# Optimization experiments

Measured on AMD Instinct MI355X. Metric: run time of the kernel, lower is better.

Reference implementation:

```python
import jax, jax.numpy as jnp
import numpy as np

TEMPERATURE = 0.07
EPS = 1e-12  # matches F.normalize eps clamp


def setup_inputs() -> dict:
    key = jax.random.key(0)
    k1, k2 = jax.random.split(key)
    B, S, D = 8, 512, 128
    return {
        "z_i": jax.random.normal(k1, (B, S, D), dtype=jnp.float32),
        "z_j": jax.random.normal(k2, (B, S, D), dtype=jnp.float32),
    }


def reference(z_i, z_j):
    D = z_i.shape[-1]
    zi = z_i.reshape(-1, D)  # [N, D]
    zj = z_j.reshape(-1, D)
    # cosine normalization (use_cosine_similarity=True)
    zi = zi / jnp.maximum(jnp.linalg.norm(zi, axis=1, keepdims=True), EPS)
    zj = zj / jnp.maximum(jnp.linalg.norm(zj, axis=1, keepdims=True), EPS)
    N = zi.shape[0]
    z = jnp.concatenate([zi, zj], axis=0)  # [2N, D]
    sim = (z @ z.T) / TEMPERATURE  # [2N, 2N]
    # denominator: logsumexp over all j != i (positives + negatives)
    diag = jnp.eye(2 * N, dtype=bool)
    lse = jax.nn.logsumexp(jnp.where(diag, -jnp.inf, sim), axis=1)  # [2N]
    # positive logit for row i is sim[i, (i+N) mod 2N] = <zi, zj>/T for both halves
    pos_half = jnp.sum(zi * zj, axis=1) / TEMPERATURE  # [N]
    pos = jnp.concatenate([pos_half, pos_half])  # [2N]
    return jnp.mean(-pos + lse)
```

## Files before the change

### kernel.cpp

```cpp
#include <hip/hip_runtime.h>
#include <stdint.h>


#define TOTAL   8192
#define NHALF   4096
#define DK      128
#define TEMP_INV 14.285714285714286f
#define SCALE    4.539816f

#define JSPLITS 16
#define JCHUNK  (TOTAL / JSPLITS)
#define BN      64
#define NSTAGE  (JCHUNK / BN)
#define BM      256

typedef short  bf16x8  __attribute__((ext_vector_type(8)));
typedef float  floatx4 __attribute__((ext_vector_type(4)));

#if __has_builtin(__builtin_amdgcn_exp2f)
#define EXP2(x) __builtin_amdgcn_exp2f(x)
#else
#define EXP2(x) exp2f(x)
#endif

__device__ __forceinline__ uint32_t f2bf(float f) {
  uint32_t u = __float_as_uint(f);
  return (u + 0x7fffu + ((u >> 16) & 1u)) >> 16;
}
__device__ __forceinline__ uint32_t pack2bf(float lo, float hi) {
  return f2bf(lo) | (f2bf(hi) << 16);
}

__global__ __launch_bounds__(256) void ntx_norm(
    const float* __restrict__ zi, const float* __restrict__ zj,
    uint32_t* __restrict__ zn,
    float* __restrict__ pos,
    float* __restrict__ rowsum)
{
  const int t = threadIdx.x;
  if (blockIdx.x < 32) rowsum[blockIdx.x * 256 + t] = 0.0f;

  const int wave = t >> 6, lane = t & 63;
  const int i = blockIdx.x * 4 + wave;

  const float2 vi = *(const float2*)(zi + (size_t)i * DK + lane * 2);
  const float2 vj = *(const float2*)(zj + (size_t)i * DK + lane * 2);
  float ssi = vi.x * vi.x + vi.y * vi.y;
  float ssj = vj.x * vj.x + vj.y * vj.y;
  float dij = vi.x * vj.x + vi.y * vj.y;
#pragma unroll
  for (int m = 1; m <= 32; m <<= 1) {
    ssi += __shfl_xor(ssi, m, 64);
    ssj += __shfl_xor(ssj, m, 64);
    dij += __shfl_xor(dij, m, 64);
  }
  const float invi = 1.0f / fmaxf(sqrtf(ssi), 1e-12f);
  const float invj = 1.0f / fmaxf(sqrtf(ssj), 1e-12f);

  zn[(size_t)i * 64 + lane] =
      pack2bf(vi.x * invi * SCALE, vi.y * invi * SCALE);
  zn[(size_t)(i + NHALF) * 64 + lane] =
      pack2bf(vj.x * invj * SCALE, vj.y * invj * SCALE);
  if (lane == 0) pos[i] = dij * invi * invj * TEMP_INV;
}

__global__ __launch_bounds__(256, 2) void ntx_gemm(
    const uint16_t* __restrict__ z,
    float* __restrict__ rowsum)
{
  __shared__ uint4 lb4[BN * 17];

  const int t = threadIdx.x;
  const int wave = t >> 6, lane = t & 63;
  const int q = lane >> 4, c = lane & 15;
  const int i0 = blockIdx.x * BM;
  const int j0 = blockIdx.y * JCHUNK;
  const int rowbase = i0 + wave * 64;

  bf16x8 afrag[4][4];
#pragma unroll
  for (int s = 0; s < 4; ++s) {
    const uint16_t* ap = z + (size_t)(rowbase + s * 16 + c) * DK + q * 8;
#pragma unroll
    for (int kk = 0; kk < 4; ++kk)
      afrag[s][kk] = *(const bf16x8*)(ap + kk * 32);
  }

  float runsum[4][4];
#pragma unroll
  for (int s = 0; s < 4; ++s)
#pragma unroll
    for (int r = 0; r < 4; ++r) runsum[s][r] = 0.0f;

  const int ch = t & 15;
  const int r0 = t >> 4;

  for (int st = 0; st < NSTAGE; ++st) {
    const int jst = j0 + st * BN;
    __syncthreads();
#pragma unroll
    for (int p = 0; p < 4; ++p) {
      const int r = r0 + p * 16;
      uint4 v = *(const uint4*)(z + (size_t)(jst + r) * DK + ch * 8);
      lb4[r * 17 + ch] = v;
    }
    __syncthreads();

#pragma unroll
    for (int jt = 0; jt < BN / 16; ++jt) {
      bf16x8 bfrag[4];
#pragma unroll
      for (int kk = 0; kk < 4; ++kk)
        bfrag[kk] = *(const bf16x8*)&lb4[(jt * 16 + c) * 17 + kk * 4 + q];
      const int jc = jst + jt * 16;

#pragma unroll
      for (int s = 0; s < 4; ++s) {
        floatx4 acc = {0.0f, 0.0f, 0.0f, 0.0f};
#pragma unroll
        for (int kk = 0; kk < 4; ++kk)
          acc = __builtin_amdgcn_mfma_f32_16x16x32_bf16(afrag[s][kk],
                                                        bfrag[kk], acc,
                                                        0, 0, 0);
        const int rb = rowbase + s * 16;
        if (jc == rb) {
#pragma unroll
          for (int r = 0; r < 4; ++r) {
            float e = EXP2(acc[r]);
            runsum[s][r] += (q * 4 + r == c) ? 0.0f : e;
          }
        } else {
#pragma unroll
          for (int r = 0; r < 4; ++r) runsum[s][r] += EXP2(acc[r]);
        }
      }
    }
  }

#pragma unroll
  for (int s = 0; s < 4; ++s)
#pragma unroll
    for (int r = 0; r < 4; ++r) {
      float v = runsum[s][r];
      v += __shfl_xor(v, 1, 64);
      v += __shfl_xor(v, 2, 64);
      v += __shfl_xor(v, 4, 64);
      v += __shfl_xor(v, 8, 64);
      runsum[s][r] = v;
    }
  if (c == 0) {
#pragma unroll
    for (int s = 0; s < 4; ++s)
#pragma unroll
      for (int r = 0; r < 4; ++r)
        atomicAdd(&rowsum[rowbase + s * 16 + q * 4 + r], runsum[s][r]);
  }
}

__global__ __launch_bounds__(1024) void ntx_final(
    const float* __restrict__ rowsum, const float* __restrict__ pos,
    float* __restrict__ out)
{
  const int t = threadIdx.x;
  float acc = 0.0f;
  for (int r = t; r < TOTAL; r += 1024) acc += __logf(rowsum[r]);
  for (int r = t; r < NHALF; r += 1024) acc -= 2.0f * pos[r];
#pragma unroll
  for (int m = 1; m <= 32; m <<= 1) acc += __shfl_xor(acc, m, 64);
  __shared__ float red[16];
  const int wave = t >> 6, lane = t & 63;
  if (lane == 0) red[wave] = acc;
  __syncthreads();
  if (t == 0) {
    float s = 0.0f;
#pragma unroll
    for (int w = 0; w < 16; ++w) s += red[w];
    out[0] = s / (float)TOTAL;
  }
}

extern "C" void kernel_launch(void* const* d_in, const int* in_sizes, int n_in,
                              void* d_out, int out_size, void* d_ws,
                              size_t ws_size, hipStream_t stream) {
  const float* zi = (const float*)d_in[0];
  const float* zj = (const float*)d_in[1];
  float* out = (float*)d_out;

  char* ws = (char*)d_ws;
  uint16_t* zn     = (uint16_t*)ws;
  float*    rowsum = (float*)(ws + (size_t)TOTAL * DK * 2);
  float*    pos    = (float*)(ws + (size_t)TOTAL * DK * 2 + TOTAL * 4);

  ntx_norm<<<dim3(NHALF / 4), dim3(256), 0, stream>>>(zi, zj, (uint32_t*)zn,
                                                      pos, rowsum);
  ntx_gemm<<<dim3(TOTAL / BM, JSPLITS), dim3(256), 0, stream>>>(zn, rowsum);
  ntx_final<<<dim3(1), dim3(1024), 0, stream>>>(rowsum, pos, out);
}
```

Baseline: 86.35 us.

## Exploit similarity-matrix symmetry: compute upper-triangle tiles and scatter column sums

The GEMM+exp kernel now uses 128x128 tiles and computes only the tiles on or above the diagonal, since the similarity matrix is symmetric. Each off-diagonal tile adds its exp values both to its own rows and, through per-column partial sums, to the mirrored rows. The goal is to roughly halve the MFMA and exp2 work. In exchange it launches a 64x64 grid where about half the blocks exit at once, does a separate LDS load and sync per small tile, and issues many more global atomics, including duplicate column atomics from each of the four waves.

```diff
diff --git a/kernel.cpp b/kernel.cpp
--- a/kernel.cpp
+++ b/kernel.cpp
@@ -7,12 +7,7 @@
 #define DK      128
 #define TEMP_INV 14.285714285714286f
 #define SCALE    4.539816f
-
-#define JSPLITS 16
-#define JCHUNK  (TOTAL / JSPLITS)
-#define BN      64
-#define NSTAGE  (JCHUNK / BN)
-#define BM      256
+#define TILE    128
 
 typedef short  bf16x8  __attribute__((ext_vector_type(8)));
 typedef float  floatx4 __attribute__((ext_vector_type(4)));
@@ -64,81 +59,84 @@
   if (lane == 0) pos[i] = dij * invi * invj * TEMP_INV;
 }
 
-__global__ __launch_bounds__(256, 2) void ntx_gemm(
+__global__ __launch_bounds__(256, 4) void ntx_gemm(
     const uint16_t* __restrict__ z,
     float* __restrict__ rowsum)
 {
-  __shared__ uint4 lb4[BN * 17];
+  const int bi = blockIdx.x, bj = blockIdx.y;
+  if (bj < bi) return;
+
+  __shared__ uint4 lb4[TILE * 17];
 
   const int t = threadIdx.x;
   const int wave = t >> 6, lane = t & 63;
   const int q = lane >> 4, c = lane & 15;
-  const int i0 = blockIdx.x * BM;
-  const int j0 = blockIdx.y * JCHUNK;
-  const int rowbase = i0 + wave * 64;
-
-  bf16x8 afrag[4][4];
-#pragma unroll
-  for (int s = 0; s < 4; ++s) {
+  const int I0 = bi * TILE, J0 = bj * TILE;
+  const int rowbase = I0 + wave * 32;
+  const bool diagblk = (bi == bj);
+
+  {
+    const int ch = t & 15, r0 = t >> 4;
+#pragma unroll
+    for (int p = 0; p < 8; ++p) {
+      const int r = r0 + p * 16;
+      lb4[r * 17 + ch] = *(const uint4*)(z + (size_t)(J0 + r) * DK + ch * 8);
+    }
+  }
+
+  bf16x8 afrag[2][4];
+#pragma unroll
+  for (int s = 0; s < 2; ++s) {
     const uint16_t* ap = z + (size_t)(rowbase + s * 16 + c) * DK + q * 8;
 #pragma unroll
     for (int kk = 0; kk < 4; ++kk)
       afrag[s][kk] = *(const bf16x8*)(ap + kk * 32);
   }
 
-  float runsum[4][4];
-#pragma unroll
-  for (int s = 0; s < 4; ++s)
-#pragma unroll
-    for (int r = 0; r < 4; ++r) runsum[s][r] = 0.0f;
-
-  const int ch = t & 15;
-  const int r0 = t >> 4;
-
-  for (int st = 0; st < NSTAGE; ++st) {
-    const int jst = j0 + st * BN;
-    __syncthreads();
-#pragma unroll
-    for (int p = 0; p < 4; ++p) {
-      const int r = r0 + p * 16;
-      uint4 v = *(const uint4*)(z + (size_t)(jst + r) * DK + ch * 8);
-      lb4[r * 17 + ch] = v;
-    }
-    __syncthreads();
-
-#pragma unroll
-    for (int jt = 0; jt < BN / 16; ++jt) {
-      bf16x8 bfrag[4];
+  float runsum[2][4] = {{0.f, 0.f, 0.f, 0.f}, {0.f, 0.f, 0.f, 0.f}};
+  float colacc[8];
+
+  __syncthreads();
+
+#pragma unroll
+  for (int jt = 0; jt < 8; ++jt) {
+    bf16x8 bfrag[4];
+#pragma unroll
+    for (int kk = 0; kk < 4; ++kk)
+      bfrag[kk] = *(const bf16x8*)&lb4[(jt * 16 + c) * 17 + kk * 4 + q];
+
+    float cpart = 0.0f;
+#pragma unroll
+    for (int s = 0; s < 2; ++s) {
+      floatx4 acc = {0.0f, 0.0f, 0.0f, 0.0f};
 #pragma unroll
       for (int kk = 0; kk < 4; ++kk)
-        bfrag[kk] = *(const bf16x8*)&lb4[(jt * 16 + c) * 17 + kk * 4 + q];
-      const int jc = jst + jt * 16;
-
-#pragma unroll
-      for (int s = 0; s < 4; ++s) {
-        floatx4 acc = {0.0f, 0.0f, 0.0f, 0.0f};
-#pragma unroll
-        for (int kk = 0; kk < 4; ++kk)
-          acc = __builtin_amdgcn_mfma_f32_16x16x32_bf16(afrag[s][kk],
-                                                        bfrag[kk], acc,
-                                                        0, 0, 0);
-        const int rb = rowbase + s * 16;
-        if (jc == rb) {
-#pragma unroll
-          for (int r = 0; r < 4; ++r) {
-            float e = EXP2(acc[r]);
-            runsum[s][r] += (q * 4 + r == c) ? 0.0f : e;
-          }
-        } else {
-#pragma unroll
-          for (int r = 0; r < 4; ++r) runsum[s][r] += EXP2(acc[r]);
+        acc = __builtin_amdgcn_mfma_f32_16x16x32_bf16(afrag[s][kk],
+                                                      bfrag[kk], acc, 0, 0, 0);
+      if (diagblk && (jt == wave * 2 + s)) {
+#pragma unroll
+        for (int r = 0; r < 4; ++r) {
+          float e = EXP2(acc[r]);
+          e = (q * 4 + r == c) ? 0.0f : e;
+          runsum[s][r] += e;
+          cpart += e;
+        }
+      } else {
+#pragma unroll
+        for (int r = 0; r < 4; ++r) {
+          float e = EXP2(acc[r]);
+          runsum[s][r] += e;
+          cpart += e;
         }
       }
     }
-  }
-
-#pragma unroll
-  for (int s = 0; s < 4; ++s)
+    cpart += __shfl_xor(cpart, 16, 64);
+    cpart += __shfl_xor(cpart, 32, 64);
+    colacc[jt] = cpart;
+  }
+
+#pragma unroll
+  for (int s = 0; s < 2; ++s)
 #pragma unroll
     for (int r = 0; r < 4; ++r) {
       float v = runsum[s][r];
@@ -150,10 +148,15 @@
     }
   if (c == 0) {
 #pragma unroll
-    for (int s = 0; s < 4; ++s)
+    for (int s = 0; s < 2; ++s)
 #pragma unroll
       for (int r = 0; r < 4; ++r)
         atomicAdd(&rowsum[rowbase + s * 16 + q * 4 + r], runsum[s][r]);
+  }
+  if (!diagblk && q == 0) {
+#pragma unroll
+    for (int jt = 0; jt < 8; ++jt)
+      atomicAdd(&rowsum[J0 + jt * 16 + c], colacc[jt]);
   }
 }
 
@@ -193,6 +196,6 @@
 
   ntx_norm<<<dim3(NHALF / 4), dim3(256), 0, stream>>>(zi, zj, (uint32_t*)zn,
                                                       pos, rowsum);
-  ntx_gemm<<<dim3(TOTAL / BM, JSPLITS), dim3(256), 0, stream>>>(zn, rowsum);
+  ntx_gemm<<<dim3(64, 64), dim3(256), 0, stream>>>(zn, rowsum);
   ntx_final<<<dim3(1), dim3(1024), 0, stream>>>(rowsum, pos, out);
 }
```

Result: slower. 93.79 us (+8.6%).
